# Performance work log

Hardware: AMD Instinct MI355X
Metric: run time of the kernel (lower is better)

The kernel has to match this reference:

```python
import jax, jax.numpy as jnp
import numpy as np

N_NODES = 50000
N_EDGES = 800000
NFEAT, NHID1, NHID2, NHID3, NCLASS = 128, 128, 128, 64, 32


def _glorot(key, fan_in, fan_out):
    lim = 1.0 / np.sqrt(fan_in)
    return jax.random.uniform(key, (fan_in, fan_out), jnp.float32, -lim, lim)


def setup_inputs() -> dict:
    key = jax.random.key(0)
    ks = jax.random.split(key, 12)
    x = jax.random.normal(ks[0], (N_NODES, NFEAT), jnp.float32)
    edge_src = jax.random.randint(ks[1], (N_EDGES,), 0, N_NODES, jnp.int32)
    edge_dst = jax.random.randint(ks[2], (N_EDGES,), 0, N_NODES, jnp.int32)
    edge_val = jax.random.uniform(ks[3], (N_EDGES,), jnp.float32)
    W1 = _glorot(ks[4], NFEAT, NHID1)
    W2 = _glorot(ks[5], NHID1, NHID2)
    W3 = _glorot(ks[6], NHID2, NHID3)
    W4 = _glorot(ks[7], NHID3, NCLASS)
    b1 = jnp.zeros((NHID1,), jnp.float32)
    b2 = jnp.zeros((NHID2,), jnp.float32)
    b3 = jnp.zeros((NHID3,), jnp.float32)
    b4 = jnp.zeros((NCLASS,), jnp.float32)
    return {"x": x, "edge_src": edge_src, "edge_dst": edge_dst, "edge_val": edge_val,
            "W1": W1, "b1": b1, "W2": W2, "b2": b2, "W3": W3, "b3": b3, "W4": W4, "b4": b4}


def _gc_layer(h, W, b, src, dst, val):
    # support = h @ W ; out = adj @ support + b  (adj in COO form)
    support = h @ W                                   # [N, d_out]
    msgs = support[src] * val[:, None]                # [E, d_out] irregular gather
    agg = jax.ops.segment_sum(msgs, dst, num_segments=N_NODES)  # scatter-add
    return agg + b


def reference(x, edge_src, edge_dst, edge_val, W1, b1, W2, b2, W3, b3, W4, b4):
    h = jax.nn.relu(_gc_layer(x, W1, b1, edge_src, edge_dst, edge_val))
    h = jax.nn.relu(_gc_layer(h, W2, b2, edge_src, edge_dst, edge_val))
    h = jax.nn.relu(_gc_layer(h, W3, b3, edge_src, edge_dst, edge_val))
    h = _gc_layer(h, W4, b4, edge_src, edge_dst, edge_val)
    return h
```

## Files before the change

kernel.cpp:

```cpp
#include <hip/hip_runtime.h>

constexpr int NNODES = 50000;
constexpr int NEDGES = 800000;
constexpr int CAP = 64;

constexpr int NPART = 8;
constexpr int PSIZE = NNODES / NPART;
constexpr int FCH = 1024;
constexpr int QCAP = 320;

constexpr int CHUNKS = (NEDGES + FCH - 1) / FCH;
constexpr int TILE_ITEMS = (NNODES + 63) / 64;
constexpr int PACK_TOT = 43008;
constexpr int PREP_ITEMS = NNODES;

typedef __attribute__((ext_vector_type(8))) short short8;
typedef __attribute__((ext_vector_type(8))) unsigned short ushort8;
typedef __attribute__((ext_vector_type(4))) float f32x4;

__device__ __forceinline__ unsigned short f2b(float f) {
    unsigned int u = __float_as_uint(f);
    u += 0x7FFFu + ((u >> 16) & 1u);
    return (unsigned short)(u >> 16);
}
__device__ __forceinline__ float b2f(unsigned short u) {
    return __uint_as_float(((unsigned int)u) << 16);
}
__device__ __forceinline__ float recval(unsigned int rec) {
    return __uint_as_float(rec & 0xFFFF0000u);
}

template <int N, int K>
__device__ __forceinline__ void pack_one(int idx, const float* __restrict__ W,
                                         unsigned short* __restrict__ Wp) {
    constexpr int KS = K / 32;
    int j = idx & 7;
    int lane = (idx >> 3) & 63;
    int t = idx >> 9;
    int nt = t / KS, ks = t % KS;
    int n = nt * 16 + (lane & 15);
    int k = ks * 32 + (lane >> 4) * 8 + j;
    Wp[idx] = f2b(W[(size_t)k * N + n]);
}

__global__ __launch_bounds__(256) void prep_kernel(
        const float* __restrict__ W1, const float* __restrict__ W2,
        const float* __restrict__ W3, const float* __restrict__ W4,
        unsigned short* __restrict__ Wp1, unsigned short* __restrict__ Wp2,
        unsigned short* __restrict__ Wp3, unsigned short* __restrict__ Wp4,
        int* __restrict__ cursor) {
    int p = blockIdx.x * 256 + threadIdx.x;
    if (p < NNODES) cursor[p] = 0;
    if (p < 16384) pack_one<128, 128>(p, W1, Wp1);
    else if (p < 32768) pack_one<128, 128>(p - 16384, W2, Wp2);
    else if (p < 40960) pack_one<64, 128>(p - 32768, W3, Wp3);
    else if (p < 43008) pack_one<32, 64>(p - 40960, W4, Wp4);
}

template <int N, int K, bool AF32>
__device__ __forceinline__ void gemm_item(int t, const void* __restrict__ Hv,
                                          const unsigned short* __restrict__ Wp,
                                          unsigned short* __restrict__ Sb) {
    constexpr int NT = N / 16, KS = K / 32;
    const int lane = threadIdx.x & 63;
    const int wave = threadIdx.x >> 6;
    const int waveRow = t * 64 + wave * 16;
    const int m = lane & 15, quad = lane >> 4;
    int arow = waveRow + m;
    if (arow >= NNODES) arow = NNODES - 1;

    f32x4 acc[NT];
#pragma unroll
    for (int nt = 0; nt < NT; ++nt) acc[nt] = (f32x4){0.f, 0.f, 0.f, 0.f};

#pragma unroll
    for (int ks = 0; ks < KS; ++ks) {
        short8 a;
        if (AF32) {
            const float* hp = (const float*)Hv + (size_t)arow * K + ks * 32 + quad * 8;
            float4 a0 = *reinterpret_cast<const float4*>(hp);
            float4 a1 = *reinterpret_cast<const float4*>(hp + 4);
            a[0] = (short)f2b(a0.x); a[1] = (short)f2b(a0.y);
            a[2] = (short)f2b(a0.z); a[3] = (short)f2b(a0.w);
            a[4] = (short)f2b(a1.x); a[5] = (short)f2b(a1.y);
            a[6] = (short)f2b(a1.z); a[7] = (short)f2b(a1.w);
        } else {
            a = *reinterpret_cast<const short8*>(
                (const unsigned short*)Hv + (size_t)arow * K + ks * 32 + quad * 8);
        }
#pragma unroll
        for (int nt = 0; nt < NT; ++nt) {
            short8 b = *reinterpret_cast<const short8*>(Wp + ((nt * KS + ks) * 64 + lane) * 8);
            acc[nt] = __builtin_amdgcn_mfma_f32_16x16x32_bf16(a, b, acc[nt], 0, 0, 0);
        }
    }

#pragma unroll
    for (int reg = 0; reg < 4; ++reg) {
        int grow = waveRow + quad * 4 + reg;
        if (grow < NNODES) {
#pragma unroll
            for (int nt = 0; nt < NT; ++nt)
                Sb[(size_t)grow * N + nt * 16 + m] = f2b(acc[nt][reg]);
        }
    }
}

__global__ __launch_bounds__(256) void fill_gemm1_kernel(
        const int* __restrict__ src, const int* __restrict__ dst,
        const float* __restrict__ val, int* __restrict__ cursor,
        unsigned int* __restrict__ buckets,
        const float* __restrict__ x, const unsigned short* __restrict__ Wp1,
        unsigned short* __restrict__ Q) {
    __shared__ unsigned int q_rec[QCAP];
    __shared__ int q_d[QCAP];
    __shared__ int qcount;

    const int g = blockIdx.x / 9;
    const int r = blockIdx.x % 9;
    if (r == 0) {
        gemm_item<128, 128, true>(g, x, Wp1, Q);
        return;
    }

    if (threadIdx.x == 0) qcount = 0;
    __syncthreads();

    const int part = blockIdx.x & 7;
    const int lo = part * PSIZE, hi = lo + PSIZE;
    const int e0 = g * FCH + threadIdx.x * 4;

    int4 d4 = make_int4(-1, -1, -1, -1);
    int4 s4 = make_int4(0, 0, 0, 0);
    float4 v4 = make_float4(0.f, 0.f, 0.f, 0.f);
    if (e0 + 3 < NEDGES) {
        d4 = *reinterpret_cast<const int4*>(dst + e0);
        s4 = *reinterpret_cast<const int4*>(src + e0);
        v4 = *reinterpret_cast<const float4*>(val + e0);
    } else if (e0 < NEDGES) {
        d4.x = dst[e0]; s4.x = src[e0]; v4.x = val[e0];
        if (e0 + 1 < NEDGES) { d4.y = dst[e0 + 1]; s4.y = src[e0 + 1]; v4.y = val[e0 + 1]; }
        if (e0 + 2 < NEDGES) { d4.z = dst[e0 + 2]; s4.z = src[e0 + 2]; v4.z = val[e0 + 2]; }
    }
    int dd[4] = {d4.x, d4.y, d4.z, d4.w};
    int ss[4] = {s4.x, s4.y, s4.z, s4.w};
    float vv[4] = {v4.x, v4.y, v4.z, v4.w};
#pragma unroll
    for (int i = 0; i < 4; ++i) {
        int d = dd[i];
        if (d >= lo && d < hi) {
            unsigned int rec = (unsigned int)ss[i] | ((unsigned int)f2b(vv[i]) << 16);
            int pos = atomicAdd(&qcount, 1);
            if (pos < QCAP) {
                q_rec[pos] = rec;
                q_d[pos] = d;
            } else {
                int p = atomicAdd(&cursor[d], 1);
                if (p < CAP) buckets[(size_t)d * CAP + p] = rec;
            }
        }
    }
    __syncthreads();

    int n = qcount < QCAP ? qcount : QCAP;
    for (int i = threadIdx.x; i < n; i += 256) {
        int d = q_d[i];
        unsigned int rec = q_rec[i];
        int p = atomicAdd(&cursor[d], 1);
        if (p < CAP) buckets[(size_t)d * CAP + p] = rec;
    }
}

template <int NIN>
__device__ __forceinline__ void pull_agg(const unsigned short* __restrict__ Sprev,
                                         const unsigned int* __restrict__ eb,
                                         int cnt, int cg, float* __restrict__ acc) {
    const unsigned short* Sp = Sprev + cg * 8;
    int j = 0;
    for (; j + 8 <= cnt; j += 8) {
        uint4 ea = *reinterpret_cast<const uint4*>(eb + j);
        uint4 ec = *reinterpret_cast<const uint4*>(eb + j + 4);
        const ushort8 m0 = *reinterpret_cast<const ushort8*>(Sp + (ea.x & 0xFFFFu) * (unsigned)NIN);
        const ushort8 m1 = *reinterpret_cast<const ushort8*>(Sp + (ea.y & 0xFFFFu) * (unsigned)NIN);
        const ushort8 m2 = *reinterpret_cast<const ushort8*>(Sp + (ea.z & 0xFFFFu) * (unsigned)NIN);
        const ushort8 m3 = *reinterpret_cast<const ushort8*>(Sp + (ea.w & 0xFFFFu) * (unsigned)NIN);
        const ushort8 m4 = *reinterpret_cast<const ushort8*>(Sp + (ec.x & 0xFFFFu) * (unsigned)NIN);
        const ushort8 m5 = *reinterpret_cast<const ushort8*>(Sp + (ec.y & 0xFFFFu) * (unsigned)NIN);
        const ushort8 m6 = *reinterpret_cast<const ushort8*>(Sp + (ec.z & 0xFFFFu) * (unsigned)NIN);
        const ushort8 m7 = *reinterpret_cast<const ushort8*>(Sp + (ec.w & 0xFFFFu) * (unsigned)NIN);
        float v0 = recval(ea.x), v1 = recval(ea.y), v2 = recval(ea.z), v3 = recval(ea.w);
        float v4 = recval(ec.x), v5 = recval(ec.y), v6 = recval(ec.z), v7 = recval(ec.w);
#pragma unroll
        for (int t = 0; t < 8; ++t) {
            acc[t] = fmaf(b2f(m0[t]), v0, acc[t]);
            acc[t] = fmaf(b2f(m1[t]), v1, acc[t]);
            acc[t] = fmaf(b2f(m2[t]), v2, acc[t]);
            acc[t] = fmaf(b2f(m3[t]), v3, acc[t]);
            acc[t] = fmaf(b2f(m4[t]), v4, acc[t]);
            acc[t] = fmaf(b2f(m5[t]), v5, acc[t]);
            acc[t] = fmaf(b2f(m6[t]), v6, acc[t]);
            acc[t] = fmaf(b2f(m7[t]), v7, acc[t]);
        }
    }
    for (; j + 4 <= cnt; j += 4) {
        uint4 ea = *reinterpret_cast<const uint4*>(eb + j);
        const ushort8 m0 = *reinterpret_cast<const ushort8*>(Sp + (ea.x & 0xFFFFu) * (unsigned)NIN);
        const ushort8 m1 = *reinterpret_cast<const ushort8*>(Sp + (ea.y & 0xFFFFu) * (unsigned)NIN);
        const ushort8 m2 = *reinterpret_cast<const ushort8*>(Sp + (ea.z & 0xFFFFu) * (unsigned)NIN);
        const ushort8 m3 = *reinterpret_cast<const ushort8*>(Sp + (ea.w & 0xFFFFu) * (unsigned)NIN);
        float v0 = recval(ea.x), v1 = recval(ea.y);
        float v2 = recval(ea.z), v3 = recval(ea.w);
#pragma unroll
        for (int t = 0; t < 8; ++t) {
            acc[t] = fmaf(b2f(m0[t]), v0, acc[t]);
            acc[t] = fmaf(b2f(m1[t]), v1, acc[t]);
            acc[t] = fmaf(b2f(m2[t]), v2, acc[t]);
            acc[t] = fmaf(b2f(m3[t]), v3, acc[t]);
        }
    }
    for (; j < cnt; ++j) {
        unsigned int r = eb[j];
        float v = recval(r);
        const ushort8 mr = *reinterpret_cast<const ushort8*>(Sp + (r & 0xFFFFu) * (unsigned)NIN);
#pragma unroll
        for (int t = 0; t < 8; ++t) acc[t] = fmaf(b2f(mr[t]), v, acc[t]);
    }
}

template <int NIN, int NOUT>
__global__ __launch_bounds__(256) void agg_gemm_kernel(
        const unsigned short* __restrict__ Sprev, const unsigned int* __restrict__ buckets,
        const int* __restrict__ counts, const float* __restrict__ bias,
        const unsigned short* __restrict__ Wp, unsigned short* __restrict__ Snext) {
    constexpr int NCH = NIN / 8;
    constexpr int R = 256 / NCH;
    constexpr int LROW = NIN + 8;
    constexpr int KS = NIN / 32;
    constexpr int NT = NOUT / 16;
    constexpr int RT = R / 16;
    constexpr int TILES = RT * NT;
    __shared__ unsigned short htile[R * LROW];

    const int nodeBase = blockIdx.x * R;

    {
        int nl = threadIdx.x / NCH;
        int cg = threadIdx.x % NCH;
        int node = nodeBase + nl;
        float acc[8];
        if (node < NNODES) {
#pragma unroll
            for (int t = 0; t < 8; ++t) acc[t] = bias[cg * 8 + t];
            int cnt = counts[node];
            if (cnt > CAP) cnt = CAP;
            pull_agg<NIN>(Sprev, buckets + (size_t)node * CAP, cnt, cg, acc);
        } else {
#pragma unroll
            for (int t = 0; t < 8; ++t) acc[t] = 0.f;
        }
        ushort8 o;
#pragma unroll
        for (int t = 0; t < 8; ++t) o[t] = f2b(fmaxf(acc[t], 0.f));
        *reinterpret_cast<ushort8*>(&htile[nl * LROW + cg * 8]) = o;
    }
    __syncthreads();

    {
        const int lane = threadIdx.x & 63, wave = threadIdx.x >> 6;
        const int m = lane & 15, quad = lane >> 4;
        for (int t = wave; t < TILES; t += 4) {
            int rt = t / NT, nt = t % NT;
            f32x4 acc = (f32x4){0.f, 0.f, 0.f, 0.f};
#pragma unroll
            for (int ks = 0; ks < KS; ++ks) {
                short8 a = *reinterpret_cast<const short8*>(
                    &htile[(rt * 16 + m) * LROW + ks * 32 + quad * 8]);
                short8 b = *reinterpret_cast<const short8*>(Wp + ((nt * KS + ks) * 64 + lane) * 8);
                acc = __builtin_amdgcn_mfma_f32_16x16x32_bf16(a, b, acc, 0, 0, 0);
            }
#pragma unroll
            for (int reg = 0; reg < 4; ++reg) {
                int grow = nodeBase + rt * 16 + quad * 4 + reg;
                if (grow < NNODES)
                    Snext[(size_t)grow * NOUT + nt * 16 + m] = f2b(acc[reg]);
            }
        }
    }
}

__global__ __launch_bounds__(256) void agg_out_kernel(const unsigned short* __restrict__ Sb,
        const unsigned int* __restrict__ buckets, const int* __restrict__ counts,
        const float* __restrict__ bias, float* __restrict__ outp) {
    constexpr int N = 32;
    int node = blockIdx.x * 64 + threadIdx.x / 4;
    int cg = threadIdx.x % 4;
    if (node >= NNODES) return;
    float acc[8];
#pragma unroll
    for (int t = 0; t < 8; ++t) acc[t] = bias[cg * 8 + t];

    int cnt = counts[node];
    if (cnt > CAP) cnt = CAP;
    pull_agg<N>(Sb, buckets + (size_t)node * CAP, cnt, cg, acc);

    float* op = outp + (size_t)node * N + cg * 8;
    *reinterpret_cast<float4*>(op) = make_float4(acc[0], acc[1], acc[2], acc[3]);
    *reinterpret_cast<float4*>(op + 4) = make_float4(acc[4], acc[5], acc[6], acc[7]);
}

extern "C" void kernel_launch(void* const* d_in, const int* in_sizes, int n_in,
                              void* d_out, int out_size, void* d_ws, size_t ws_size,
                              hipStream_t stream) {
    const float* x   = (const float*)d_in[0];
    const int*   src = (const int*)d_in[1];
    const int*   dst = (const int*)d_in[2];
    const float* val = (const float*)d_in[3];
    const float* W1  = (const float*)d_in[4];
    const float* b1  = (const float*)d_in[5];
    const float* W2  = (const float*)d_in[6];
    const float* b2  = (const float*)d_in[7];
    const float* W3  = (const float*)d_in[8];
    const float* b3  = (const float*)d_in[9];
    const float* W4  = (const float*)d_in[10];
    const float* b4  = (const float*)d_in[11];
    float* out = (float*)d_out;

    unsigned short* P = (unsigned short*)d_ws;
    unsigned short* Q = P + (size_t)NNODES * 128;
    unsigned int* buckets = (unsigned int*)(Q + (size_t)NNODES * 128);
    unsigned short* Wp1 = (unsigned short*)(buckets + (size_t)NNODES * CAP);
    unsigned short* Wp2 = Wp1 + 128 * 128;
    unsigned short* Wp3 = Wp2 + 128 * 128;
    unsigned short* Wp4 = Wp3 + 128 * 64;
    int* cursor = (int*)(Wp4 + 64 * 32);

    const dim3 blk(256);

    prep_kernel<<<(PREP_ITEMS + 255) / 256, blk, 0, stream>>>(
        W1, W2, W3, W4, Wp1, Wp2, Wp3, Wp4, cursor);
    fill_gemm1_kernel<<<CHUNKS * 9, blk, 0, stream>>>(
        src, dst, val, cursor, buckets, x, Wp1, Q);
    agg_gemm_kernel<128, 128><<<(NNODES + 15) / 16, blk, 0, stream>>>(
        Q, buckets, cursor, b1, Wp2, P);
    agg_gemm_kernel<128, 64><<<(NNODES + 15) / 16, blk, 0, stream>>>(
        P, buckets, cursor, b2, Wp3, Q);
    agg_gemm_kernel<64, 32><<<(NNODES + 31) / 32, blk, 0, stream>>>(
        Q, buckets, cursor, b3, Wp4, P);
    agg_out_kernel<<<(NNODES + 63) / 64, blk, 0, stream>>>(P, buckets, cursor, b4, out);
}
```

Baseline: 217.2 us.

## Build edge buckets per node slice with shared-memory cursors instead of global atomics

The edge bucketing now gives each of 64 blocks a contiguous slice of destination nodes. Each block scans the whole dst array and appends matching edges using per-node cursors held in shared memory, then writes the final counts to global memory. This removes the global atomic cursors, the overflow queue and the cursor zeroing in the prep kernel. In exchange every slice block re-reads the full dst array, and only 64 blocks do all the bucketing work, which may leave that part latency-bound.

```diff
diff --git a/kernel.cpp b/kernel.cpp
--- a/kernel.cpp
+++ b/kernel.cpp
@@ -4,15 +4,10 @@
 constexpr int NEDGES = 800000;
 constexpr int CAP = 64;
 
-constexpr int NPART = 8;
-constexpr int PSIZE = NNODES / NPART;
-constexpr int FCH = 1024;
-constexpr int QCAP = 320;
-
-constexpr int CHUNKS = (NEDGES + FCH - 1) / FCH;
+constexpr int NSLICE = 64;
+constexpr int SL = (NNODES + NSLICE - 1) / NSLICE;
 constexpr int TILE_ITEMS = (NNODES + 63) / 64;
 constexpr int PACK_TOT = 43008;
-constexpr int PREP_ITEMS = NNODES;
 
 typedef __attribute__((ext_vector_type(8))) short short8;
 typedef __attribute__((ext_vector_type(8))) unsigned short ushort8;
@@ -47,10 +42,8 @@
         const float* __restrict__ W1, const float* __restrict__ W2,
         const float* __restrict__ W3, const float* __restrict__ W4,
         unsigned short* __restrict__ Wp1, unsigned short* __restrict__ Wp2,
-        unsigned short* __restrict__ Wp3, unsigned short* __restrict__ Wp4,
-        int* __restrict__ cursor) {
+        unsigned short* __restrict__ Wp3, unsigned short* __restrict__ Wp4) {
     int p = blockIdx.x * 256 + threadIdx.x;
-    if (p < NNODES) cursor[p] = 0;
     if (p < 16384) pack_one<128, 128>(p, W1, Wp1);
     else if (p < 32768) pack_one<128, 128>(p - 16384, W2, Wp2);
     else if (p < 40960) pack_one<64, 128>(p - 32768, W3, Wp3);
@@ -112,63 +105,41 @@
         unsigned int* __restrict__ buckets,
         const float* __restrict__ x, const unsigned short* __restrict__ Wp1,
         unsigned short* __restrict__ Q) {
-    __shared__ unsigned int q_rec[QCAP];
-    __shared__ int q_d[QCAP];
-    __shared__ int qcount;
-
-    const int g = blockIdx.x / 9;
-    const int r = blockIdx.x % 9;
-    if (r == 0) {
-        gemm_item<128, 128, true>(g, x, Wp1, Q);
+    __shared__ int lcur[SL];
+
+    if (blockIdx.x >= NSLICE) {
+        gemm_item<128, 128, true>(blockIdx.x - NSLICE, x, Wp1, Q);
         return;
     }
 
-    if (threadIdx.x == 0) qcount = 0;
+    const int b = blockIdx.x;
+    const int nlo = b * SL;
+    const int nn = (NNODES - nlo < SL) ? (NNODES - nlo) : SL;
+    for (int i = threadIdx.x; i < nn; i += 256) lcur[i] = 0;
     __syncthreads();
 
-    const int part = blockIdx.x & 7;
-    const int lo = part * PSIZE, hi = lo + PSIZE;
-    const int e0 = g * FCH + threadIdx.x * 4;
-
-    int4 d4 = make_int4(-1, -1, -1, -1);
-    int4 s4 = make_int4(0, 0, 0, 0);
-    float4 v4 = make_float4(0.f, 0.f, 0.f, 0.f);
-    if (e0 + 3 < NEDGES) {
-        d4 = *reinterpret_cast<const int4*>(dst + e0);
-        s4 = *reinterpret_cast<const int4*>(src + e0);
-        v4 = *reinterpret_cast<const float4*>(val + e0);
-    } else if (e0 < NEDGES) {
-        d4.x = dst[e0]; s4.x = src[e0]; v4.x = val[e0];
-        if (e0 + 1 < NEDGES) { d4.y = dst[e0 + 1]; s4.y = src[e0 + 1]; v4.y = val[e0 + 1]; }
-        if (e0 + 2 < NEDGES) { d4.z = dst[e0 + 2]; s4.z = src[e0 + 2]; v4.z = val[e0 + 2]; }
-    }
-    int dd[4] = {d4.x, d4.y, d4.z, d4.w};
-    int ss[4] = {s4.x, s4.y, s4.z, s4.w};
-    float vv[4] = {v4.x, v4.y, v4.z, v4.w};
-#pragma unroll
-    for (int i = 0; i < 4; ++i) {
-        int d = dd[i];
-        if (d >= lo && d < hi) {
-            unsigned int rec = (unsigned int)ss[i] | ((unsigned int)f2b(vv[i]) << 16);
-            int pos = atomicAdd(&qcount, 1);
-            if (pos < QCAP) {
-                q_rec[pos] = rec;
-                q_d[pos] = d;
-            } else {
-                int p = atomicAdd(&cursor[d], 1);
-                if (p < CAP) buckets[(size_t)d * CAP + p] = rec;
+    const int tid = threadIdx.x;
+    for (int base = 0; base < NEDGES; base += 2048) {
+        const int e0 = base + tid * 8;
+        if (e0 + 8 <= NEDGES) {
+            int4 d0 = *reinterpret_cast<const int4*>(dst + e0);
+            int4 d1 = *reinterpret_cast<const int4*>(dst + e0 + 4);
+            int darr[8] = {d0.x, d0.y, d0.z, d0.w, d1.x, d1.y, d1.z, d1.w};
+#pragma unroll
+            for (int k = 0; k < 8; ++k) {
+                unsigned int rel = (unsigned int)(darr[k] - nlo);
+                if (rel < (unsigned int)nn) {
+                    int e = e0 + k;
+                    unsigned int rec = (unsigned int)src[e] |
+                                       ((unsigned int)f2b(val[e]) << 16);
+                    int p = atomicAdd(&lcur[rel], 1);
+                    if (p < CAP) buckets[(size_t)darr[k] * CAP + p] = rec;
+                }
             }
         }
     }
     __syncthreads();
-
-    int n = qcount < QCAP ? qcount : QCAP;
-    for (int i = threadIdx.x; i < n; i += 256) {
-        int d = q_d[i];
-        unsigned int rec = q_rec[i];
-        int p = atomicAdd(&cursor[d], 1);
-        if (p < CAP) buckets[(size_t)d * CAP + p] = rec;
-    }
+    for (int i = threadIdx.x; i < nn; i += 256) cursor[nlo + i] = lcur[i];
 }
 
 template <int NIN>
@@ -336,9 +307,9 @@
 
     const dim3 blk(256);
 
-    prep_kernel<<<(PREP_ITEMS + 255) / 256, blk, 0, stream>>>(
-        W1, W2, W3, W4, Wp1, Wp2, Wp3, Wp4, cursor);
-    fill_gemm1_kernel<<<CHUNKS * 9, blk, 0, stream>>>(
+    prep_kernel<<<(PACK_TOT + 255) / 256, blk, 0, stream>>>(
+        W1, W2, W3, W4, Wp1, Wp2, Wp3, Wp4);
+    fill_gemm1_kernel<<<NSLICE + TILE_ITEMS, blk, 0, stream>>>(
         src, dst, val, cursor, buckets, x, Wp1, Q);
     agg_gemm_kernel<128, 128><<<(NNODES + 15) / 16, blk, 0, stream>>>(
         Q, buckets, cursor, b1, Wp2, P);
```

Measured after the change: 836.1 us. +284.9%, slower.

## Split 128-wide aggregation into column slices pinned per XCD, separate GEMMs

Applied to the files above, without the earlier changes.

Stores the 128-wide intermediate features in a column-sliced layout (four slices of 32 columns, each spanning all nodes). Aggregation for layers 1 and 2 now runs in a dedicated slice kernel whose block-to-XCD mapping pins each slice to particular XCDs, so each XCD's L2 only holds a 3.2 MB slice of the gather source. The dense GEMMs for those layers become standalone kernels that read and write the sliced layout. This aims to improve gather cache hit rates at the cost of two extra kernel launches and an extra round-trip of the aggregated activations through global memory.

```diff
diff --git a/kernel.cpp b/kernel.cpp
--- a/kernel.cpp
+++ b/kernel.cpp
@@ -13,6 +13,7 @@
 constexpr int TILE_ITEMS = (NNODES + 63) / 64;
 constexpr int PACK_TOT = 43008;
 constexpr int PREP_ITEMS = NNODES;
+constexpr int AGG_CHUNK2 = 391;
 
 typedef __attribute__((ext_vector_type(8))) short short8;
 typedef __attribute__((ext_vector_type(8))) unsigned short ushort8;
@@ -57,7 +58,7 @@
     else if (p < 43008) pack_one<32, 64>(p - 40960, W4, Wp4);
 }
 
-template <int N, int K, bool AF32>
+template <int N, int K, int AMODE, bool CSLICE>
 __device__ __forceinline__ void gemm_item(int t, const void* __restrict__ Hv,
                                           const unsigned short* __restrict__ Wp,
                                           unsigned short* __restrict__ Sb) {
@@ -76,7 +77,7 @@
 #pragma unroll
     for (int ks = 0; ks < KS; ++ks) {
         short8 a;
-        if (AF32) {
+        if (AMODE == 0) {
             const float* hp = (const float*)Hv + (size_t)arow * K + ks * 32 + quad * 8;
             float4 a0 = *reinterpret_cast<const float4*>(hp);
             float4 a1 = *reinterpret_cast<const float4*>(hp + 4);
@@ -86,7 +87,7 @@
             a[6] = (short)f2b(a1.z); a[7] = (short)f2b(a1.w);
         } else {
             a = *reinterpret_cast<const short8*>(
-                (const unsigned short*)Hv + (size_t)arow * K + ks * 32 + quad * 8);
+                (const unsigned short*)Hv + ((size_t)ks * NNODES + arow) * 32 + quad * 8);
         }
 #pragma unroll
         for (int nt = 0; nt < NT; ++nt) {
@@ -100,8 +101,13 @@
         int grow = waveRow + quad * 4 + reg;
         if (grow < NNODES) {
 #pragma unroll
-            for (int nt = 0; nt < NT; ++nt)
-                Sb[(size_t)grow * N + nt * 16 + m] = f2b(acc[nt][reg]);
+            for (int nt = 0; nt < NT; ++nt) {
+                int c = nt * 16 + m;
+                if (CSLICE)
+                    Sb[((size_t)(c >> 5) * NNODES + grow) * 32 + (c & 31)] = f2b(acc[nt][reg]);
+                else
+                    Sb[(size_t)grow * N + c] = f2b(acc[nt][reg]);
+            }
         }
     }
 }
@@ -119,7 +125,7 @@
     const int g = blockIdx.x / 9;
     const int r = blockIdx.x % 9;
     if (r == 0) {
-        gemm_item<128, 128, true>(g, x, Wp1, Q);
+        gemm_item<128, 128, 0, true>(g, x, Wp1, Q);
         return;
     }
 
@@ -227,11 +233,45 @@
     }
 }
 
-template <int NIN, int NOUT>
-__global__ __launch_bounds__(256) void agg_gemm_kernel(
+__global__ __launch_bounds__(256) void agg_slice_kernel(
+        const unsigned short* __restrict__ Sprev, const unsigned int* __restrict__ buckets,
+        const int* __restrict__ counts, const float* __restrict__ bias,
+        unsigned short* __restrict__ Hout) {
+    const int xcd = blockIdx.x & 7;
+    const int ss = xcd & 3;
+    const int sub = xcd >> 2;
+    const int chunk = (blockIdx.x >> 3) * 2 + sub;
+    const int nl = threadIdx.x >> 2;
+    const int cg = threadIdx.x & 3;
+    const int node = chunk * 64 + nl;
+    if (node >= NNODES) return;
+
+    float acc[8];
+#pragma unroll
+    for (int t = 0; t < 8; ++t) acc[t] = bias[ss * 32 + cg * 8 + t];
+    int cnt = counts[node];
+    if (cnt > CAP) cnt = CAP;
+    pull_agg<32>(Sprev + (size_t)ss * NNODES * 32, buckets + (size_t)node * CAP,
+                 cnt, cg, acc);
+
+    ushort8 o;
+#pragma unroll
+    for (int t = 0; t < 8; ++t) o[t] = f2b(fmaxf(acc[t], 0.f));
+    *reinterpret_cast<ushort8*>(Hout + ((size_t)ss * NNODES + node) * 32 + cg * 8) = o;
+}
+
+template <int N, bool CSLICE>
+__global__ __launch_bounds__(256) void gemm_sb_kernel(
+        const unsigned short* __restrict__ A, const unsigned short* __restrict__ Wp,
+        unsigned short* __restrict__ C) {
+    gemm_item<N, 128, 1, CSLICE>(blockIdx.x, A, Wp, C);
+}
+
+__global__ __launch_bounds__(256) void agg_gemm64_kernel(
         const unsigned short* __restrict__ Sprev, const unsigned int* __restrict__ buckets,
         const int* __restrict__ counts, const float* __restrict__ bias,
         const unsigned short* __restrict__ Wp, unsigned short* __restrict__ Snext) {
+    constexpr int NIN = 64, NOUT = 32;
     constexpr int NCH = NIN / 8;
     constexpr int R = 256 / NCH;
     constexpr int LROW = NIN + 8;
@@ -325,9 +365,9 @@
     const float* b4  = (const float*)d_in[11];
     float* out = (float*)d_out;
 
-    unsigned short* P = (unsigned short*)d_ws;
-    unsigned short* Q = P + (size_t)NNODES * 128;
-    unsigned int* buckets = (unsigned int*)(Q + (size_t)NNODES * 128);
+    unsigned short* B1 = (unsigned short*)d_ws;
+    unsigned short* B2 = B1 + (size_t)NNODES * 128;
+    unsigned int* buckets = (unsigned int*)(B2 + (size_t)NNODES * 128);
     unsigned short* Wp1 = (unsigned short*)(buckets + (size_t)NNODES * CAP);
     unsigned short* Wp2 = Wp1 + 128 * 128;
     unsigned short* Wp3 = Wp2 + 128 * 128;
@@ -339,12 +379,14 @@
     prep_kernel<<<(PREP_ITEMS + 255) / 256, blk, 0, stream>>>(
         W1, W2, W3, W4, Wp1, Wp2, Wp3, Wp4, cursor);
     fill_gemm1_kernel<<<CHUNKS * 9, blk, 0, stream>>>(
-        src, dst, val, cursor, buckets, x, Wp1, Q);
-    agg_gemm_kernel<128, 128><<<(NNODES + 15) / 16, blk, 0, stream>>>(
-        Q, buckets, cursor, b1, Wp2, P);
-    agg_gemm_kernel<128, 64><<<(NNODES + 15) / 16, blk, 0, stream>>>(
-        P, buckets, cursor, b2, Wp3, Q);
-    agg_gemm_kernel<64, 32><<<(NNODES + 31) / 32, blk, 0, stream>>>(
-        Q, buckets, cursor, b3, Wp4, P);
-    agg_out_kernel<<<(NNODES + 63) / 64, blk, 0, stream>>>(P, buckets, cursor, b4, out);
-}
+        src, dst, val, cursor, buckets, x, Wp1, B1);
+    agg_slice_kernel<<<AGG_CHUNK2 * 8, blk, 0, stream>>>(
+        B1, buckets, cursor, b1, B2);
+    gemm_sb_kernel<128, true><<<TILE_ITEMS, blk, 0, stream>>>(B2, Wp2, B1);
+    agg_slice_kernel<<<AGG_CHUNK2 * 8, blk, 0, stream>>>(
+        B1, buckets, cursor, b2, B2);
+    gemm_sb_kernel<64, false><<<TILE_ITEMS, blk, 0, stream>>>(B2, Wp3, B1);
+    agg_gemm64_kernel<<<(NNODES + 31) / 32, blk, 0, stream>>>(
+        B1, buckets, cursor, b3, Wp4, B2);
+    agg_out_kernel<<<(NNODES + 63) / 64, blk, 0, stream>>>(B2, buckets, cursor, b4, out);
+}
```

Result: slower. 238.3 us (+9.7%).
